# Optimization experiments

Hardware: AMD Instinct MI355X
Metric: run time of the kernel (lower is better)

## Reference

```python
import jax, jax.numpy as jnp
import numpy as np

EPS = 1e-8
TEMP = 0.2
HOPS = 2


def _inv_sqrt_deg(deg):
    # deg^-0.5 with inf -> 0 (isolated nodes)
    return jnp.where(deg > 0, jax.lax.rsqrt(jnp.maximum(deg, 1.0)) * jnp.where(deg > 0, 1.0, 0.0), 0.0)


def gcn_conv(h, u, v, W, b, n):
    # PyG GCNConv: add self-loops, symmetric normalization, aggr='add'
    h = h @ W  # [N, out]
    loops = jnp.arange(n, dtype=u.dtype)
    uu = jnp.concatenate([u, loops])
    vv = jnp.concatenate([v, loops])
    deg = jax.ops.segment_sum(jnp.ones_like(vv, dtype=h.dtype), vv, num_segments=n)
    dis = _inv_sqrt_deg(deg)
    norm = dis[uu] * dis[vv]  # [E+N]
    out = jax.ops.segment_sum(norm[:, None] * h[uu], vv, num_segments=n)
    return out + b


def compute_message_passing(u, v, x, n, hop=HOPS):
    # to_undirected: concat edges with their flips; remove self-loops via mask
    uu = jnp.concatenate([u, v])
    vv = jnp.concatenate([v, u])
    mask = (uu != vv).astype(x.dtype)
    deg = jax.ops.segment_sum(mask, vv, num_segments=n)
    dis = _inv_sqrt_deg(deg)
    norm = dis[uu] * dis[vv] * mask  # zero out self-loop edges
    for _ in range(hop):
        x = jax.ops.segment_sum(norm[:, None] * x[uu], vv, num_segments=n)
    return x


def _cos_sim(a, b):
    na = jnp.maximum(jnp.sqrt(jnp.sum(a * a, axis=-1)), EPS)
    nb = jnp.maximum(jnp.sqrt(jnp.sum(b * b, axis=-1)), EPS)
    return jnp.sum(a * b, axis=-1) / (na * nb)


def setup_inputs() -> dict:
    key = jax.random.key(0)
    ks = jax.random.split(key, 10)
    N, E, B = 100_000, 800_000, 100_000
    Din, H, Dout = 256, 256, 64
    x = jax.random.normal(ks[0], (N, Din), dtype=jnp.float32)
    src = jax.random.randint(ks[1], (E,), 0, N, dtype=jnp.int32)
    off = jax.random.randint(ks[2], (E,), 1, N, dtype=jnp.int32)
    dst = (src + off) % N  # guaranteed no self-loops
    edge_index = jnp.stack([src, dst])  # [2, E]
    batch = jax.random.randint(ks[3], (B, 3), 0, N, dtype=jnp.int32)
    s1, s2, sp = 1.0 / np.sqrt(Din), 1.0 / np.sqrt(H), 1.0 / np.sqrt(H)
    W1 = jax.random.normal(ks[4], (Din, H), dtype=jnp.float32) * s1
    b1 = jnp.zeros((H,), jnp.float32)
    W2 = jax.random.normal(ks[5], (H, H), dtype=jnp.float32) * s2
    b2 = jnp.zeros((H,), jnp.float32)
    Wp = jax.random.normal(ks[6], (H, Dout), dtype=jnp.float32) * sp
    bp = jnp.zeros((Dout,), jnp.float32)
    return {"x": x, "edge_index": edge_index, "batch": batch,
            "W1": W1, "b1": b1, "W2": W2, "b2": b2, "Wp": Wp, "bp": bp}


def reference(x, edge_index, batch, W1, b1, W2, b2, Wp, bp):
    n = x.shape[0]
    u, v = edge_index[0], edge_index[1]
    # gnn_encoder: 2-layer GCN
    h = jax.nn.relu(gcn_conv(x, u, v, W1, b1, n))
    h = gcn_conv(h, u, v, W2, b2, n)
    # graph_pred_linear
    node_emb = h @ Wp + bp  # [N, Dout]
    # 2-hop degree-normalized propagation on the undirected graph
    all_emb = compute_message_passing(u, v, node_emb, n)
    anc = all_emb[batch[:, 0]]
    pos = all_emb[batch[:, 1]]
    neg = all_emb[batch[:, 2]]
    xs = jnp.exp(_cos_sim(anc, pos) / TEMP)
    ys = jnp.exp(_cos_sim(anc, neg) / TEMP)
    loss = -jnp.log(xs / (xs + ys))
    return loss.mean()
```

## Files before the change

kernel.cpp:

```cpp
#include <hip/hip_runtime.h>
#include <hip/hip_bf16.h>

#define DIN 256
#define HID 256
#define DOUT 64
#define NPART 8
#define FPB 128
#define CCAP 32

typedef short short8 __attribute__((ext_vector_type(8)));
typedef float f32x4 __attribute__((ext_vector_type(4)));
typedef float f32x2 __attribute__((ext_vector_type(2)));

__device__ __forceinline__ float b2f(ushort u) {
    unsigned int x = ((unsigned int)u) << 16;
    return __builtin_bit_cast(float, x);
}
__device__ __forceinline__ ushort f2bf(float f) {
    unsigned int u = __builtin_bit_cast(unsigned int, f);
    unsigned int r = (u + 0x7FFFu + ((u >> 16) & 1u)) >> 16;
    return (ushort)r;
}
__device__ __forceinline__ unsigned int cvt_pk(float lo, float hi) {
    unsigned int r;
    asm("v_cvt_pk_bf16_f32 %0, %1, %2" : "=v"(r) : "v"(lo), "v"(hi));
    return r;
}
__device__ __forceinline__ unsigned char f2fp8(float v) {
    int p = __builtin_amdgcn_cvt_pk_fp8_f32(v, v, 0, false);
    return (unsigned char)(p & 0xff);
}
__device__ __forceinline__ ushort f2fp8x2(float lo, float hi) {
    int p = __builtin_amdgcn_cvt_pk_fp8_f32(lo, hi, 0, false);
    return (ushort)(p & 0xffff);
}
__device__ __forceinline__ void gload16(const void* g, void* l) {
    __builtin_amdgcn_global_load_lds(
        (const __attribute__((address_space(1))) unsigned int*)g,
        (__attribute__((address_space(3))) unsigned int*)l, 16, 0, 0);
}
__device__ __forceinline__ int swz8(int lane, int r) {
    return (((lane >> 1) ^ (r & 7)) << 4) + (lane & 1) * 8;
}

__device__ __forceinline__ void fill_body(int fid,
                                          const int* __restrict__ u,
                                          const int* __restrict__ v,
                                          int* __restrict__ cnt_in,
                                          int* __restrict__ cnt_out,
                                          int* __restrict__ col_in,
                                          int* __restrict__ col_out,
                                          int E, unsigned pdiv) {
    const int part = fid & (NPART - 1);
    const int step = FPB * 512;
    int e = (fid >> 3) * 512 + threadIdx.x;

#define PROC(aa, bb)                                                  \
    do {                                                              \
        if ((unsigned)(bb) / pdiv == (unsigned)part) {                \
            int s_ = atomicAdd(&cnt_in[bb], 1);                       \
            if (s_ < CCAP) col_in[(bb) * CCAP + s_] = (aa);           \
        }                                                             \
        if ((unsigned)(aa) / pdiv == (unsigned)part) {                \
            int s_ = atomicAdd(&cnt_out[aa], 1);                      \
            if (s_ < CCAP) col_out[(aa) * CCAP + s_] = (bb);          \
        }                                                             \
    } while (0)

    for (; e + 3 * step < E; e += 4 * step) {
        int a0 = u[e],            b0 = v[e];
        int a1 = u[e + step],     b1 = v[e + step];
        int a2 = u[e + 2 * step], b2 = v[e + 2 * step];
        int a3 = u[e + 3 * step], b3 = v[e + 3 * step];
        PROC(a0, b0);
        PROC(a1, b1);
        PROC(a2, b2);
        PROC(a3, b3);
    }
    for (; e < E; e += step) {
        int a = u[e], b = v[e];
        PROC(a, b);
    }
#undef PROC
}

template <int NT, int TN, int OUTMODE, bool ADD_BIAS, bool A_F32, bool SCALE>
__device__ __forceinline__ void gemm_body(
    int bidx, char* As, char* Bs,
    const void* __restrict__ A, const char* __restrict__ Bt,
    const float* __restrict__ bias, const float* __restrict__ rowscale,
    void* __restrict__ C, int M) {
    constexpr int BM = 64;
    constexpr int TILES = NT / TN;
    constexpr int FM = (TN == 128) ? 2 : 1;
    constexpr int FN = 2;
    const int tid = threadIdx.x;
    const int w = tid >> 6;
    const int lane = tid & 63;
    const int row0 = bidx * BM;
    const int wrow = (TN == 128) ? ((w >> 2) * 32) : ((w >> 1) * 16);
    const int wcol = (TN == 128) ? ((w & 3) * 32) : ((w & 1) * 32);
    const int g = lane >> 4;
    const int r15 = lane & 15;
    const int wb = w * 1024;

    if (A_F32) {
        const float* Af = (const float*)A;
        int r = tid >> 3;
        int c8 = tid & 7;
        int gr = row0 + r;
        gr = (gr < M) ? gr : (M - 1);
        const float* src = Af + (size_t)gr * 256 + c8 * 8;
#pragma unroll
        for (int k = 0; k < 4; ++k) {
            float4 f0 = *(const float4*)(src + k * 64);
            float4 f1 = *(const float4*)(src + k * 64 + 4);
            uint4 pv;
            pv.x = cvt_pk(f0.x, f0.y);
            pv.y = cvt_pk(f0.z, f0.w);
            pv.z = cvt_pk(f1.x, f1.y);
            pv.w = cvt_pk(f1.z, f1.w);
            int chunk = (c8 + 8 * k) ^ (r & 7);
            *(uint4*)(As + r * 512 + (chunk << 4)) = pv;
        }
    } else {
        const char* gA = (const char*)A + (size_t)row0 * 512;
#pragma unroll
        for (int i = 0; i < BM / 16; ++i)
            gload16(gA + i * 8192 + wb + lane * 16, As + i * 8192 + wb);
    }
    {
        const char* gB = Bt;
#pragma unroll
        for (int i = 0; i < TN / 16; ++i)
            gload16(gB + i * 8192 + wb + lane * 16, Bs + i * 8192 + wb);
    }

#pragma unroll
    for (int t = 0; t < TILES; ++t) {
        __syncthreads();

        f32x4 acc[FM][FN];
#pragma unroll
        for (int m = 0; m < FM; ++m)
#pragma unroll
            for (int n = 0; n < FN; ++n) acc[m][n] = {0.f, 0.f, 0.f, 0.f};

#pragma unroll
        for (int ks = 0; ks < 8; ++ks) {
            short8 a[FM], b[FN];
#pragma unroll
            for (int m = 0; m < FM; ++m) {
                int rl = wrow + m * 16 + r15;
                a[m] = *(const short8*)(As + rl * 512 + (((ks * 4 + g) ^ (rl & 7)) << 4));
            }
#pragma unroll
            for (int n = 0; n < FN; ++n) {
                int cl = wcol + n * 16 + r15;
                b[n] = *(const short8*)(Bs + cl * 512 + (((ks * 4 + g) ^ (cl & 7)) << 4));
            }
#pragma unroll
            for (int m = 0; m < FM; ++m)
#pragma unroll
                for (int n = 0; n < FN; ++n)
                    acc[m][n] = __builtin_amdgcn_mfma_f32_16x16x32_bf16(a[m], b[n], acc[m][n], 0, 0, 0);
        }

        __syncthreads();
        if (t + 1 < TILES) {
            const char* gB = Bt + (size_t)((t + 1) * TN) * 512;
#pragma unroll
            for (int i = 0; i < TN / 16; ++i)
                gload16(gB + i * 8192 + wb + lane * 16, Bs + i * 8192 + wb);
        }

#pragma unroll
        for (int m = 0; m < FM; ++m) {
            int rbase = row0 + wrow + m * 16 + g * 4;
#pragma unroll
            for (int j = 0; j < 4; ++j) {
                int grow = rbase + j;
                if (grow >= M) continue;
                float rs = SCALE ? rowscale[grow] : 1.0f;
#pragma unroll
                for (int n = 0; n < FN; ++n) {
                    int gcol = t * TN + wcol + n * 16 + r15;
                    float vv = acc[m][n][j];
                    if (ADD_BIAS) vv += bias[gcol];
                    if (SCALE) vv *= rs;
                    if (OUTMODE == 2)
                        ((unsigned char*)C)[(size_t)grow * 256 + gcol] = f2fp8(vv);
                    else
                        ((unsigned char*)C)[(size_t)grow * 64 + gcol] = f2fp8(vv);
                }
            }
        }
    }
}

__global__ __launch_bounds__(512) void fill_gemm1_kernel(
    const int* __restrict__ u, const int* __restrict__ v,
    int* __restrict__ cnt_in, int* __restrict__ cnt_out,
    int* __restrict__ col_in, int* __restrict__ col_out,
    int E, unsigned pdiv,
    const float* __restrict__ x, const char* __restrict__ w1t,
    unsigned char* __restrict__ hb, int M,
    int gG, int gF, int nG, int nF) {
    __shared__ __align__(16) char As[64 * 512];
    __shared__ __align__(16) char Bs[64 * 512];
    const int G = blockIdx.x >> 3;
    const int sub = blockIdx.x & 7;
    const int gmin = (gG < gF) ? gG : gF;
    bool isG;
    int idx;
    if (G < 2 * gmin) {
        isG = ((G & 1) == 0);
        idx = (G >> 1) * 8 + sub;
    } else if (gG > gF) {
        isG = true;
        idx = (G - gmin) * 8 + sub;
    } else {
        isG = false;
        idx = (G - gmin) * 8 + sub;
    }
    if (isG) {
        if (idx < nG)
            gemm_body<256, 64, 2, false, true, false>(idx, As, Bs, x, w1t,
                                                      nullptr, nullptr, hb, M);
    } else {
        if (idx < nF)
            fill_body(idx, u, v, cnt_in, cnt_out, col_in, col_out, E, pdiv);
    }
}

template <int NT, int TN, int OUTMODE, bool ADD_BIAS, bool A_F32>
__global__ __launch_bounds__(512) void mfma_gemm_v7(
    const void* __restrict__ A, const char* __restrict__ Bt,
    const float* __restrict__ bias, const float* __restrict__ rowscale,
    void* __restrict__ C, int M) {
    __shared__ __align__(16) char As[64 * 512];
    __shared__ __align__(16) char Bs[TN * 512];
    gemm_body<NT, TN, OUTMODE, ADD_BIAS, A_F32, true>(
        blockIdx.x, As, Bs, A, Bt, bias, rowscale, C, M);
}

__global__ __launch_bounds__(256) void wcast_kernel(
    const float* __restrict__ W1, const float* __restrict__ W2,
    const float* __restrict__ Wp,
    char* __restrict__ w1t, char* __restrict__ w2t, char* __restrict__ wpt) {
    int row = blockIdx.x;
    const float* W; char* Wt; int NOUT;
    if (row < 256)      { W = W1; Wt = w1t; NOUT = 256; }
    else if (row < 512) { W = W2; Wt = w2t; NOUT = 256; row -= 256; }
    else                { W = Wp; Wt = wpt; NOUT = 64;  row -= 512; }
    int k = threadIdx.x;
    *(ushort*)(Wt + (size_t)row * 512 + (((k >> 3) ^ (row & 7)) << 4) + (k & 7) * 2)
        = f2bf(W[k * NOUT + row]);
}

__global__ __launch_bounds__(256) void dis_kernel(const int* __restrict__ cnt_in,
                                                  const int* __restrict__ cnt_out,
                                                  float* __restrict__ dis_g,
                                                  float* __restrict__ dis_m,
                                                  int N) {
    int i = blockIdx.x * blockDim.x + threadIdx.x;
    if (i >= N) return;
    int ci = cnt_in[i];
    dis_g[i] = rsqrtf((float)ci + 1.0f);
    int dm = ci + cnt_out[i];
    dis_m[i] = (dm > 0) ? rsqrtf((float)dm) : 0.0f;
}

template <bool RELU, bool NEIGH_DIS>
__global__ __launch_bounds__(256) void conv_gather_fp8(const unsigned char* __restrict__ h,
                                                       const float* __restrict__ dis,
                                                       const float* __restrict__ bias,
                                                       const int* __restrict__ cnt_in,
                                                       const int* __restrict__ col_in,
                                                       char* __restrict__ out,
                                                       int N) {
    int wid = (blockIdx.x * blockDim.x + threadIdx.x) >> 6;
    int lane = threadIdx.x & 63;
    if (wid >= N) return;
    float di = dis[wid];
    float a0, a1, a2, a3;
    {
        unsigned q = *(const unsigned*)(h + (size_t)wid * 256 + lane * 4);
        f32x2 lo = __builtin_amdgcn_cvt_pk_f32_fp8((int)q, false);
        f32x2 hi = __builtin_amdgcn_cvt_pk_f32_fp8((int)q, true);
        float ws = NEIGH_DIS ? di : 1.0f;
        a0 = ws * lo.x; a1 = ws * lo.y; a2 = ws * hi.x; a3 = ws * hi.y;
    }
    const int* list = col_in + (size_t)wid * CCAP;
    int cnt = cnt_in[wid];
    cnt = (cnt < CCAP) ? cnt : CCAP;
    int e = 0;
    for (; e + 7 < cnt; e += 8) {
        int ss[8];
        unsigned qs[8];
#pragma unroll
        for (int k = 0; k < 8; ++k) ss[k] = list[e + k];
#pragma unroll
        for (int k = 0; k < 8; ++k)
            qs[k] = *(const unsigned*)(h + (size_t)ss[k] * 256 + lane * 4);
#pragma unroll
        for (int k = 0; k < 8; ++k) {
            float wgt = NEIGH_DIS ? dis[ss[k]] : 1.0f;
            f32x2 lo = __builtin_amdgcn_cvt_pk_f32_fp8((int)qs[k], false);
            f32x2 hi = __builtin_amdgcn_cvt_pk_f32_fp8((int)qs[k], true);
            a0 += wgt * lo.x; a1 += wgt * lo.y;
            a2 += wgt * hi.x; a3 += wgt * hi.y;
        }
    }
    for (; e < cnt; ++e) {
        int s = list[e];
        float wgt = NEIGH_DIS ? dis[s] : 1.0f;
        unsigned q = *(const unsigned*)(h + (size_t)s * 256 + lane * 4);
        f32x2 lo = __builtin_amdgcn_cvt_pk_f32_fp8((int)q, false);
        f32x2 hi = __builtin_amdgcn_cvt_pk_f32_fp8((int)q, true);
        a0 += wgt * lo.x; a1 += wgt * lo.y;
        a2 += wgt * hi.x; a3 += wgt * hi.y;
    }
    float4 bv = ((const float4*)bias)[lane];
    float o0 = di * a0 + bv.x;
    float o1 = di * a1 + bv.y;
    float o2 = di * a2 + bv.z;
    float o3 = di * a3 + bv.w;
    if (RELU) {
        o0 = fmaxf(o0, 0.f); o1 = fmaxf(o1, 0.f);
        o2 = fmaxf(o2, 0.f); o3 = fmaxf(o3, 0.f);
    }
    uint2 ov;
    ov.x = cvt_pk(o0, o1);
    ov.y = cvt_pk(o2, o3);
    *(uint2*)(out + (size_t)wid * 512 + swz8(lane, wid)) = ov;
}

template <int POW>
__global__ __launch_bounds__(256) void mp_gather_fp8(const unsigned char* __restrict__ in,
                                                     const float* __restrict__ dis,
                                                     const int* __restrict__ cnt_in,
                                                     const int* __restrict__ cnt_out,
                                                     const int* __restrict__ col_in,
                                                     const int* __restrict__ col_out,
                                                     unsigned char* __restrict__ out,
                                                     int N) {
    int wid = (blockIdx.x * blockDim.x + threadIdx.x) >> 6;
    int lane = threadIdx.x & 63;
    if (wid >= N) return;
    const int half = lane >> 5;
    const int l2 = lane & 31;
    const int* list;
    int cnt;
    if (half == 0) {
        list = col_in + (size_t)wid * CCAP;
        cnt = cnt_in[wid];
    } else {
        list = col_out + (size_t)wid * CCAP;
        cnt = cnt_out[wid];
    }
    cnt = (cnt < CCAP) ? cnt : CCAP;
    float a0 = 0.f, a1 = 0.f;
    int e = 0;
    for (; e + 3 < cnt; e += 4) {
        int s0 = list[e], s1 = list[e + 1], s2 = list[e + 2], s3 = list[e + 3];
        ushort q0 = *(const ushort*)(in + (size_t)s0 * 64 + l2 * 2);
        ushort q1 = *(const ushort*)(in + (size_t)s1 * 64 + l2 * 2);
        ushort q2 = *(const ushort*)(in + (size_t)s2 * 64 + l2 * 2);
        ushort q3 = *(const ushort*)(in + (size_t)s3 * 64 + l2 * 2);
        f32x2 f0 = __builtin_amdgcn_cvt_pk_f32_fp8((int)q0, false);
        f32x2 f1 = __builtin_amdgcn_cvt_pk_f32_fp8((int)q1, false);
        f32x2 f2 = __builtin_amdgcn_cvt_pk_f32_fp8((int)q2, false);
        f32x2 f3 = __builtin_amdgcn_cvt_pk_f32_fp8((int)q3, false);
        a0 += f0.x + f1.x + f2.x + f3.x;
        a1 += f0.y + f1.y + f2.y + f3.y;
    }
    for (; e < cnt; ++e) {
        int s = list[e];
        ushort q = *(const ushort*)(in + (size_t)s * 64 + l2 * 2);
        f32x2 f = __builtin_amdgcn_cvt_pk_f32_fp8((int)q, false);
        a0 += f.x;
        a1 += f.y;
    }
    a0 += __shfl_xor(a0, 32);
    a1 += __shfl_xor(a1, 32);
    if (half == 0) {
        float d = dis[wid];
        float sc = (POW == 2) ? d * d : d;
        *(ushort*)(out + (size_t)wid * 64 + l2 * 2) = f2fp8x2(sc * a0, sc * a1);
    }
}

__global__ __launch_bounds__(256) void loss_kernel(const unsigned char* __restrict__ emb,
                                                   const int* __restrict__ batch,
                                                   float* __restrict__ out,
                                                   int B, float invB) {
    const int nhw = gridDim.x * 8;
    const int hwid = blockIdx.x * 8 + (threadIdx.x >> 5);
    const int l2 = threadIdx.x & 31;
    float lsum = 0.0f;
    for (int r = hwid; r < B; r += nhw) {
        int a = batch[r * 3 + 0];
        int p = batch[r * 3 + 1];
        int ng = batch[r * 3 + 2];
        ushort qa = *(const ushort*)(emb + (size_t)a * 64 + l2 * 2);
        ushort qp = *(const ushort*)(emb + (size_t)p * 64 + l2 * 2);
        ushort qn = *(const ushort*)(emb + (size_t)ng * 64 + l2 * 2);
        f32x2 fa = __builtin_amdgcn_cvt_pk_f32_fp8((int)qa, false);
        f32x2 fp = __builtin_amdgcn_cvt_pk_f32_fp8((int)qp, false);
        f32x2 fn = __builtin_amdgcn_cvt_pk_f32_fp8((int)qn, false);
        float aa = fa.x * fa.x + fa.y * fa.y;
        float pp = fp.x * fp.x + fp.y * fp.y;
        float nn = fn.x * fn.x + fn.y * fn.y;
        float ap = fa.x * fp.x + fa.y * fp.y;
        float an = fa.x * fn.x + fa.y * fn.y;
#pragma unroll
        for (int off = 16; off > 0; off >>= 1) {
            aa += __shfl_xor(aa, off);
            pp += __shfl_xor(pp, off);
            nn += __shfl_xor(nn, off);
            ap += __shfl_xor(ap, off);
            an += __shfl_xor(an, off);
        }
        if (l2 == 0) {
            float na = fmaxf(sqrtf(aa), 1e-8f);
            float npp = fmaxf(sqrtf(pp), 1e-8f);
            float nnn = fmaxf(sqrtf(nn), 1e-8f);
            float cx = ap / (na * npp);
            float cy = an / (na * nnn);
            lsum += log1pf(expf((cy - cx) * 5.0f));
        }
    }
    __shared__ float part[8];
    if (l2 == 0) part[threadIdx.x >> 5] = lsum;
    __syncthreads();
    if (threadIdx.x == 0) {
        float s = 0.f;
#pragma unroll
        for (int i = 0; i < 8; ++i) s += part[i];
        atomicAdd(out, s * invB);
    }
}

extern "C" void kernel_launch(void* const* d_in, const int* in_sizes, int n_in,
                              void* d_out, int out_size, void* d_ws, size_t ws_size,
                              hipStream_t stream) {
    const float* x   = (const float*)d_in[0];
    const int* ei    = (const int*)d_in[1];
    const int* batch = (const int*)d_in[2];
    const float* W1  = (const float*)d_in[3];
    const float* b1  = (const float*)d_in[4];
    const float* W2  = (const float*)d_in[5];
    const float* b2  = (const float*)d_in[6];
    const float* Wp  = (const float*)d_in[7];
    const float* bp  = (const float*)d_in[8];
    const int N = in_sizes[0] / DIN;
    const int E = in_sizes[1] / 2;
    const int B = in_sizes[2] / 3;
    const int* u = ei;
    const int* v = ei + E;
    const unsigned pdiv = (unsigned)((N + NPART - 1) / NPART);

    char* aggb    = (char*)d_ws;
    unsigned char* hb = (unsigned char*)(aggb + (size_t)N * 512);
    unsigned char* embA = hb + (size_t)N * 256;
    unsigned char* embB = embA + (size_t)N * 64;
    char* w1t     = (char*)(embB + (size_t)N * 64);
    char* w2t     = w1t + 256 * 512;
    char* wpt     = w2t + 256 * 512;
    float* dis_g  = (float*)(wpt + 64 * 512);
    float* dis_m  = dis_g + N;
    int* cnt_in   = (int*)(dis_m + N);
    int* cnt_out  = cnt_in + N;
    int* col_in   = cnt_out + N;
    int* col_out  = col_in + (size_t)N * CCAP;

    const int nwb = (N + 3) / 4;
    const int ndisb = (N + 255) / 256;
    const int gm = (N + 63) / 64;

    hipMemsetAsync(cnt_in, 0, 2 * (size_t)N * sizeof(int), stream);
    wcast_kernel<<<576, 256, 0, stream>>>(W1, W2, Wp, w1t, w2t, wpt);

    const int nG = gm;
    const int gG = (nG + 7) / 8;
    const int nF = NPART * FPB;
    const int gF = nF / 8;
    fill_gemm1_kernel<<<(gG + gF) * 8, 512, 0, stream>>>(
        u, v, cnt_in, cnt_out, col_in, col_out, E, pdiv,
        x, w1t, hb, N, gG, gF, nG, nF);

    dis_kernel<<<ndisb, 256, 0, stream>>>(cnt_in, cnt_out, dis_g, dis_m, N);

    conv_gather_fp8<true, true><<<nwb, 256, 0, stream>>>(
        hb, dis_g, b1, cnt_in, col_in, aggb, N);

    mfma_gemm_v7<256, 128, 2, false, false><<<gm, 512, 0, stream>>>(
        aggb, w2t, nullptr, dis_g, hb, N);
    conv_gather_fp8<false, false><<<nwb, 256, 0, stream>>>(
        hb, dis_g, b2, cnt_in, col_in, aggb, N);

    mfma_gemm_v7<64, 64, 3, true, false><<<gm, 512, 0, stream>>>(
        aggb, wpt, bp, dis_m, embA, N);

    mp_gather_fp8<2><<<nwb, 256, 0, stream>>>(embA, dis_m, cnt_in, cnt_out,
                                              col_in, col_out, embB, N);
    mp_gather_fp8<1><<<nwb, 256, 0, stream>>>(embB, dis_m, cnt_in, cnt_out,
                                              col_in, col_out, embA, N);

    hipMemsetAsync(d_out, 0, sizeof(float), stream);
    loss_kernel<<<1024, 256, 0, stream>>>(embA, batch, (float*)d_out, B, 1.0f / (float)B);
}
```

Baseline: 433.5 us.

## Fold W2·Wp into one weight and aggregate 64-dim projections for conv2

```diff
diff --git a/kernel.cpp b/kernel.cpp
--- a/kernel.cpp
+++ b/kernel.cpp
@@ -244,18 +244,45 @@
         blockIdx.x, As, Bs, A, Bt, bias, rowscale, C, M);
 }
 
-__global__ __launch_bounds__(256) void wcast_kernel(
+__global__ __launch_bounds__(256) void wprep_kernel(
     const float* __restrict__ W1, const float* __restrict__ W2,
-    const float* __restrict__ Wp,
-    char* __restrict__ w1t, char* __restrict__ w2t, char* __restrict__ wpt) {
-    int row = blockIdx.x;
-    const float* W; char* Wt; int NOUT;
-    if (row < 256)      { W = W1; Wt = w1t; NOUT = 256; }
-    else if (row < 512) { W = W2; Wt = w2t; NOUT = 256; row -= 256; }
-    else                { W = Wp; Wt = wpt; NOUT = 64;  row -= 512; }
+    const float* __restrict__ Wp, const float* __restrict__ b2,
+    const float* __restrict__ bp,
+    char* __restrict__ w1t, char* __restrict__ wct, float* __restrict__ c2) {
+    int blk = blockIdx.x;
     int k = threadIdx.x;
-    *(ushort*)(Wt + (size_t)row * 512 + (((k >> 3) ^ (row & 7)) << 4) + (k & 7) * 2)
-        = f2bf(W[k * NOUT + row]);
+    if (blk < 256) {
+        int row = blk;
+        *(ushort*)(w1t + (size_t)row * 512 + (((k >> 3) ^ (row & 7)) << 4) + (k & 7) * 2)
+            = f2bf(W1[k * 256 + row]);
+        return;
+    }
+    if (blk < 320) {
+        int c = blk - 256;
+        const float* w2row = W2 + (size_t)k * 256;
+        float s0 = 0.f, s1 = 0.f, s2 = 0.f, s3 = 0.f;
+        float s4 = 0.f, s5 = 0.f, s6 = 0.f, s7 = 0.f;
+#pragma unroll 4
+        for (int j = 0; j < 256; j += 8) {
+            s0 += w2row[j + 0] * Wp[(j + 0) * 64 + c];
+            s1 += w2row[j + 1] * Wp[(j + 1) * 64 + c];
+            s2 += w2row[j + 2] * Wp[(j + 2) * 64 + c];
+            s3 += w2row[j + 3] * Wp[(j + 3) * 64 + c];
+            s4 += w2row[j + 4] * Wp[(j + 4) * 64 + c];
+            s5 += w2row[j + 5] * Wp[(j + 5) * 64 + c];
+            s6 += w2row[j + 6] * Wp[(j + 6) * 64 + c];
+            s7 += w2row[j + 7] * Wp[(j + 7) * 64 + c];
+        }
+        float dot = ((s0 + s1) + (s2 + s3)) + ((s4 + s5) + (s6 + s7));
+        *(ushort*)(wct + (size_t)c * 512 + (((k >> 3) ^ (c & 7)) << 4) + (k & 7) * 2)
+            = f2bf(dot);
+        return;
+    }
+    if (k < 64) {
+        float s = 0.f;
+        for (int j = 0; j < 256; ++j) s += b2[j] * Wp[j * 64 + k];
+        c2[k] = s + bp[k];
+    }
 }
 
 __global__ __launch_bounds__(256) void dis_kernel(const int* __restrict__ cnt_in,
@@ -271,7 +298,6 @@
     dis_m[i] = (dm > 0) ? rsqrtf((float)dm) : 0.0f;
 }
 
-template <bool RELU, bool NEIGH_DIS>
 __global__ __launch_bounds__(256) void conv_gather_fp8(const unsigned char* __restrict__ h,
                                                        const float* __restrict__ dis,
                                                        const float* __restrict__ bias,
@@ -288,8 +314,7 @@
         unsigned q = *(const unsigned*)(h + (size_t)wid * 256 + lane * 4);
         f32x2 lo = __builtin_amdgcn_cvt_pk_f32_fp8((int)q, false);
         f32x2 hi = __builtin_amdgcn_cvt_pk_f32_fp8((int)q, true);
-        float ws = NEIGH_DIS ? di : 1.0f;
-        a0 = ws * lo.x; a1 = ws * lo.y; a2 = ws * hi.x; a3 = ws * hi.y;
+        a0 = di * lo.x; a1 = di * lo.y; a2 = di * hi.x; a3 = di * hi.y;
     }
     const int* list = col_in + (size_t)wid * CCAP;
     int cnt = cnt_in[wid];
@@ -305,7 +330,7 @@
             qs[k] = *(const unsigned*)(h + (size_t)ss[k] * 256 + lane * 4);
 #pragma unroll
         for (int k = 0; k < 8; ++k) {
-            float wgt = NEIGH_DIS ? dis[ss[k]] : 1.0f;
+            float wgt = dis[ss[k]];
             f32x2 lo = __builtin_amdgcn_cvt_pk_f32_fp8((int)qs[k], false);
             f32x2 hi = __builtin_amdgcn_cvt_pk_f32_fp8((int)qs[k], true);
             a0 += wgt * lo.x; a1 += wgt * lo.y;
@@ -314,7 +339,7 @@
     }
     for (; e < cnt; ++e) {
         int s = list[e];
-        float wgt = NEIGH_DIS ? dis[s] : 1.0f;
+        float wgt = dis[s];
         unsigned q = *(const unsigned*)(h + (size_t)s * 256 + lane * 4);
         f32x2 lo = __builtin_amdgcn_cvt_pk_f32_fp8((int)q, false);
         f32x2 hi = __builtin_amdgcn_cvt_pk_f32_fp8((int)q, true);
@@ -322,18 +347,68 @@
         a2 += wgt * hi.x; a3 += wgt * hi.y;
     }
     float4 bv = ((const float4*)bias)[lane];
-    float o0 = di * a0 + bv.x;
-    float o1 = di * a1 + bv.y;
-    float o2 = di * a2 + bv.z;
-    float o3 = di * a3 + bv.w;
-    if (RELU) {
-        o0 = fmaxf(o0, 0.f); o1 = fmaxf(o1, 0.f);
-        o2 = fmaxf(o2, 0.f); o3 = fmaxf(o3, 0.f);
-    }
+    float o0 = fmaxf(di * a0 + bv.x, 0.f);
+    float o1 = fmaxf(di * a1 + bv.y, 0.f);
+    float o2 = fmaxf(di * a2 + bv.z, 0.f);
+    float o3 = fmaxf(di * a3 + bv.w, 0.f);
     uint2 ov;
     ov.x = cvt_pk(o0, o1);
     ov.y = cvt_pk(o2, o3);
     *(uint2*)(out + (size_t)wid * 512 + swz8(lane, wid)) = ov;
+}
+
+__global__ __launch_bounds__(256) void conv2proj_gather(const unsigned char* __restrict__ q,
+                                                        const float* __restrict__ dis_g,
+                                                        const float* __restrict__ dis_m,
+                                                        const float* __restrict__ c2,
+                                                        const int* __restrict__ cnt_in,
+                                                        const int* __restrict__ col_in,
+                                                        unsigned char* __restrict__ out,
+                                                        int N) {
+    int wid = (blockIdx.x * blockDim.x + threadIdx.x) >> 6;
+    int lane = threadIdx.x & 63;
+    if (wid >= N) return;
+    const int half = lane >> 5;
+    const int l2 = lane & 31;
+    const int* list = col_in + (size_t)wid * CCAP;
+    int cnt = cnt_in[wid];
+    cnt = (cnt < CCAP) ? cnt : CCAP;
+    float a0 = 0.f, a1 = 0.f;
+    int e = half;
+    for (; e + 6 < cnt; e += 8) {
+        int s0 = list[e], s1 = list[e + 2], s2 = list[e + 4], s3 = list[e + 6];
+        ushort q0 = *(const ushort*)(q + (size_t)s0 * 64 + l2 * 2);
+        ushort q1 = *(const ushort*)(q + (size_t)s1 * 64 + l2 * 2);
+        ushort q2 = *(const ushort*)(q + (size_t)s2 * 64 + l2 * 2);
+        ushort q3 = *(const ushort*)(q + (size_t)s3 * 64 + l2 * 2);
+        f32x2 f0 = __builtin_amdgcn_cvt_pk_f32_fp8((int)q0, false);
+        f32x2 f1 = __builtin_amdgcn_cvt_pk_f32_fp8((int)q1, false);
+        f32x2 f2 = __builtin_amdgcn_cvt_pk_f32_fp8((int)q2, false);
+        f32x2 f3 = __builtin_amdgcn_cvt_pk_f32_fp8((int)q3, false);
+        a0 += f0.x + f1.x + f2.x + f3.x;
+        a1 += f0.y + f1.y + f2.y + f3.y;
+    }
+    for (; e < cnt; e += 2) {
+        int s = list[e];
+        ushort qq = *(const ushort*)(q + (size_t)s * 64 + l2 * 2);
+        f32x2 f = __builtin_amdgcn_cvt_pk_f32_fp8((int)qq, false);
+        a0 += f.x;
+        a1 += f.y;
+    }
+    if (half == 0) {
+        ushort qq = *(const ushort*)(q + (size_t)wid * 64 + l2 * 2);
+        f32x2 f = __builtin_amdgcn_cvt_pk_f32_fp8((int)qq, false);
+        a0 += f.x;
+        a1 += f.y;
+    }
+    a0 += __shfl_xor(a0, 32);
+    a1 += __shfl_xor(a1, 32);
+    if (half == 0) {
+        float dg = dis_g[wid], dm = dis_m[wid];
+        float cA = c2[l2 * 2], cB = c2[l2 * 2 + 1];
+        *(ushort*)(out + (size_t)wid * 64 + l2 * 2) =
+            f2fp8x2(dm * (dg * a0 + cA), dm * (dg * a1 + cB));
+    }
 }
 
 template <int POW>
@@ -466,9 +541,9 @@
     unsigned char* embA = hb + (size_t)N * 256;
     unsigned char* embB = embA + (size_t)N * 64;
     char* w1t     = (char*)(embB + (size_t)N * 64);
-    char* w2t     = w1t + 256 * 512;
-    char* wpt     = w2t + 256 * 512;
-    float* dis_g  = (float*)(wpt + 64 * 512);
+    char* wct     = w1t + 256 * 512;
+    float* c2     = (float*)(wct + 64 * 512);
+    float* dis_g  = c2 + 64;
     float* dis_m  = dis_g + N;
     int* cnt_in   = (int*)(dis_m + N);
     int* cnt_out  = cnt_in + N;
@@ -480,7 +555,7 @@
     const int gm = (N + 63) / 64;
 
     hipMemsetAsync(cnt_in, 0, 2 * (size_t)N * sizeof(int), stream);
-    wcast_kernel<<<576, 256, 0, stream>>>(W1, W2, Wp, w1t, w2t, wpt);
+    wprep_kernel<<<321, 256, 0, stream>>>(W1, W2, Wp, b2, bp, w1t, wct, c2);
 
     const int nG = gm;
     const int gG = (nG + 7) / 8;
@@ -492,16 +567,13 @@
 
     dis_kernel<<<ndisb, 256, 0, stream>>>(cnt_in, cnt_out, dis_g, dis_m, N);
 
-    conv_gather_fp8<true, true><<<nwb, 256, 0, stream>>>(
-        hb, dis_g, b1, cnt_in, col_in, aggb, N);
-
-    mfma_gemm_v7<256, 128, 2, false, false><<<gm, 512, 0, stream>>>(
-        aggb, w2t, nullptr, dis_g, hb, N);
-    conv_gather_fp8<false, false><<<nwb, 256, 0, stream>>>(
-        hb, dis_g, b2, cnt_in, col_in, aggb, N);
-
-    mfma_gemm_v7<64, 64, 3, true, false><<<gm, 512, 0, stream>>>(
-        aggb, wpt, bp, dis_m, embA, N);
+    conv_gather_fp8<<<nwb, 256, 0, stream>>>(hb, dis_g, b1, cnt_in, col_in, aggb, N);
+
+    mfma_gemm_v7<64, 64, 3, false, false><<<gm, 512, 0, stream>>>(
+        aggb, wct, nullptr, dis_g, embB, N);
+
+    conv2proj_gather<<<nwb, 256, 0, stream>>>(embB, dis_g, dis_m, c2,
+                                              cnt_in, col_in, embA, N);
 
     mp_gather_fp8<2><<<nwb, 256, 0, stream>>>(embA, dis_m, cnt_in, cnt_out,
                                               col_in, col_out, embB, N);
```

New measurement: 372.8 us. -14.0%, faster.
